# Optimization experiments

Hardware: AMD Instinct MI355X
Metric: run time of the kernel (lower is better)

## Reference

```python
import jax, jax.numpy as jnp
import numpy as np

B, D, N = 131072, 512, 101
BIG = 1e9
NORM_EPS = 0.1  # F.normalize eps


def setup_inputs() -> dict:
    key = jax.random.key(0)
    k1, k2, k3 = jax.random.split(key, 3)
    embeddings = jax.random.normal(k1, (B, D), dtype=jnp.float32)
    centers_weight = jax.random.normal(k2, (N, D), dtype=jnp.float32)
    labels = jax.random.randint(k3, (B,), 0, N, dtype=jnp.int64)
    return {"embeddings": embeddings, "centers_weight": centers_weight, "labels": labels}


def reference(embeddings, centers_weight, labels):
    # ---- center (MSE) term: per-sample squared distance to own center ----
    gathered = centers_weight[labels]                     # [B, D]
    center_loss = ((embeddings - gathered) ** 2).sum(axis=1)  # [B] (reduction=None)

    # ---- margin term (original operates on .data -> detached) ----
    W = jax.lax.stop_gradient(centers_weight)
    norms = jnp.sqrt((W * W).sum(axis=1, keepdims=True))
    C = W / jnp.maximum(norms, NORM_EPS)                  # F.normalize(p=2, eps=0.1)
    n = C.shape[0]
    dist = 1.0 - C @ C.T                                  # [N, N] cosine distance
    idx = jnp.arange(n)
    diff = jnp.abs(idx[:, None] - idx[None, :])
    dist = dist + BIG * (diff == 0)                       # mask diagonal (eye)

    # neighbor distances BEFORE they are masked out
    d_lower = jnp.diagonal(dist, offset=-1)               # Dist[i, i-1], i = 1..n-1
    d_upper = jnp.diagonal(dist, offset=1)                # Dist[i, i+1], i = 0..n-2

    dist_masked = dist + BIG * (diff == 1)                # mask adjacent centers
    min_dist = dist_masked.min(axis=1)                    # Dist[i, NegIdx]

    margin = (jax.nn.relu(2.0 * d_lower - min_dist[1:]).sum()
              + jax.nn.relu(2.0 * d_upper - min_dist[:-1]).sum()) / n

    return margin + center_loss.mean()
```

## Files before the change

kernel.cpp:

```cpp
#include <hip/hip_runtime.h>

#define BB 131072
#define DD 512
#define NN 101
#define D4 128
#define HALF 64
#define NBLK 256
#define BTHR 1024
#define SPB 1024
#define NPAIR (NN * NN)
#define PPB 80

typedef float f4 __attribute__((ext_vector_type(4)));

__global__ __launch_bounds__(BTHR, 1) void fused_kernel(
    const f4* __restrict__ emb, const f4* __restrict__ ctr,
    const int* __restrict__ labels,
    float* __restrict__ partial,
    float* __restrict__ G0,
    float* __restrict__ G1)
{
    __shared__ f4  sctr[NN * HALF];
    __shared__ int slab[SPB];
    __shared__ float wsum[16];

    int b    = blockIdx.x;
    int h    = b >> 7;
    int blk  = b & 127;
    int tid  = threadIdx.x;
    int wid  = tid >> 6;
    int lane = tid & 63;

    for (int idx = tid; idx < NN * HALF; idx += BTHR) {
        int row = idx >> 6;
        int c   = idx & 63;
        sctr[idx] = ctr[row * D4 + h * HALF + c];
    }
    slab[tid] = labels[blk * SPB + tid];
    __syncthreads();

    float* Gh = h ? G1 : G0;
#pragma unroll
    for (int rep = 0; rep < 5; rep++) {
        int p = blk * PPB + rep * 16 + wid;
        if (p < NPAIR) {
            int i = p / NN;
            int j = p % NN;
            f4 a = sctr[i * HALF + lane];
            f4 c = sctr[j * HALF + lane];
            float dot = a.x * c.x + a.y * c.y + a.z * c.z + a.w * c.w;
            for (int off = 32; off > 0; off >>= 1)
                dot += __shfl_down(dot, off);
            if (lane == 0) Gh[p] = dot;
        }
    }

    float local = 0.f;
#pragma unroll 1
    for (int kk = 0; kk < 16; kk++) {
        int q0 = (kk * 4 + 0) * 16 + wid;
        int q1 = (kk * 4 + 1) * 16 + wid;
        int q2 = (kk * 4 + 2) * 16 + wid;
        int q3 = (kk * 4 + 3) * 16 + wid;
        int l0 = slab[q0];
        int l1 = slab[q1];
        int l2 = slab[q2];
        int l3 = slab[q3];
        const f4* base = emb + h * HALF + lane;
        f4 e0 = __builtin_nontemporal_load(base + (blk * SPB + q0) * D4);
        f4 e1 = __builtin_nontemporal_load(base + (blk * SPB + q1) * D4);
        f4 e2 = __builtin_nontemporal_load(base + (blk * SPB + q2) * D4);
        f4 e3 = __builtin_nontemporal_load(base + (blk * SPB + q3) * D4);
        f4 c0 = sctr[l0 * HALF + lane];
        f4 c1 = sctr[l1 * HALF + lane];
        f4 c2 = sctr[l2 * HALF + lane];
        f4 c3 = sctr[l3 * HALF + lane];
        f4 t0 = e0 - c0;
        f4 t1 = e1 - c1;
        f4 t2 = e2 - c2;
        f4 t3 = e3 - c3;
        local += t0.x * t0.x + t0.y * t0.y + t0.z * t0.z + t0.w * t0.w;
        local += t1.x * t1.x + t1.y * t1.y + t1.z * t1.z + t1.w * t1.w;
        local += t2.x * t2.x + t2.y * t2.y + t2.z * t2.z + t2.w * t2.w;
        local += t3.x * t3.x + t3.y * t3.y + t3.z * t3.z + t3.w * t3.w;
    }
    for (int off = 32; off > 0; off >>= 1)
        local += __shfl_down(local, off);
    if (lane == 0) wsum[wid] = local;
    __syncthreads();
    if (tid == 0) {
        float s = 0.f;
#pragma unroll
        for (int w = 0; w < 16; w++) s += wsum[w];
        partial[b] = s;
    }
}

__global__ __launch_bounds__(256) void finalize_kernel(
    const float* __restrict__ G0, const float* __restrict__ G1,
    const float* __restrict__ partial, float* __restrict__ out)
{
    int t = threadIdx.x;

    double dsum = (t < NBLK) ? (double)partial[t] : 0.0;
    for (int off = 32; off > 0; off >>= 1)
        dsum += __shfl_down(dsum, off);
    __shared__ double dacc[4];
    if ((t & 63) == 0) dacc[t >> 6] = dsum;

    __shared__ float denom[NN];
    __shared__ float mind[NN];
    if (t < NN)
        denom[t] = fmaxf(sqrtf(G0[t * NN + t] + G1[t * NN + t]), 0.1f);
    __syncthreads();
    if (t < NN) {
        float di = denom[t];
        float mn = 1e30f;
        for (int j = 0; j < NN; j++) {
            if (j >= t - 1 && j <= t + 1) continue;
            float g = G0[t * NN + j] + G1[t * NN + j];
            float d = 1.0f - g / (di * denom[j]);
            mn = fminf(mn, d);
        }
        mind[t] = mn;
    }
    __syncthreads();
    float contrib = 0.f;
    if (t >= 1 && t < NN) {
        float g = G0[t * NN + (t - 1)] + G1[t * NN + (t - 1)];
        float dl = 1.0f - g / (denom[t] * denom[t - 1]);
        contrib += fmaxf(2.0f * dl - mind[t], 0.0f);
    }
    if (t < NN - 1) {
        float g = G0[t * NN + (t + 1)] + G1[t * NN + (t + 1)];
        float du = 1.0f - g / (denom[t] * denom[t + 1]);
        contrib += fmaxf(2.0f * du - mind[t], 0.0f);
    }
    for (int off = 32; off > 0; off >>= 1)
        contrib += __shfl_down(contrib, off);
    __shared__ float wsum2[4];
    if ((t & 63) == 0) wsum2[t >> 6] = contrib;
    __syncthreads();
    if (t == 0) {
        float margin = (wsum2[0] + wsum2[1] + wsum2[2] + wsum2[3]) / (float)NN;
        double center = (dacc[0] + dacc[1] + dacc[2] + dacc[3]) / (double)BB;
        out[0] = margin + (float)center;
    }
}

extern "C" void kernel_launch(void* const* d_in, const int* in_sizes, int n_in,
                              void* d_out, int out_size, void* d_ws, size_t ws_size,
                              hipStream_t stream) {
    const float* emb    = (const float*)d_in[0];
    const float* ctr    = (const float*)d_in[1];
    const int*   labels = (const int*)d_in[2];
    float* out = (float*)d_out;

    float* partial = (float*)d_ws;
    float* G0      = (float*)((char*)d_ws + 1024);
    float* G1      = G0 + NPAIR;

    fused_kernel<<<NBLK, BTHR, 0, stream>>>(
        (const f4*)emb, (const f4*)ctr, labels, partial, G0, G1);
    finalize_kernel<<<1, 256, 0, stream>>>(G0, G1, partial, out);
}
```

Measured before the change: 80.54 us.

## Fold finalize into main kernel via last-block atomic counter; reorder center loop first

Removes the second kernel launch by having each block atomically increment a counter after writing its partial sum and Gram entries; the last block to arrive runs the margin and final reduction. The streaming center-loss loop is also moved ahead of the Gram dot products so the global loads are issued earlier. This saves a launch and the gap between kernels, at the cost of extra fences and an atomic per block. The counter relies on wrapping modulo 256 across calls because it is never reset.

```diff
diff --git a/kernel.cpp b/kernel.cpp
--- a/kernel.cpp
+++ b/kernel.cpp
@@ -18,11 +18,18 @@
     const int* __restrict__ labels,
     float* __restrict__ partial,
     float* __restrict__ G0,
-    float* __restrict__ G1)
+    float* __restrict__ G1,
+    unsigned int* __restrict__ done,
+    float* __restrict__ out)
 {
     __shared__ f4  sctr[NN * HALF];
     __shared__ int slab[SPB];
     __shared__ float wsum[16];
+    __shared__ unsigned int gate;
+    __shared__ double dacc[4];
+    __shared__ float denom[NN];
+    __shared__ float mind[NN];
+    __shared__ float wsum2[16];
 
     int b    = blockIdx.x;
     int h    = b >> 7;
@@ -31,13 +38,40 @@
     int wid  = tid >> 6;
     int lane = tid & 63;
 
-    for (int idx = tid; idx < NN * HALF; idx += BTHR) {
-        int row = idx >> 6;
-        int c   = idx & 63;
-        sctr[idx] = ctr[row * D4 + h * HALF + c];
-    }
+    for (int idx = tid; idx < NN * HALF; idx += BTHR)
+        sctr[idx] = ctr[(idx >> 6) * D4 + h * HALF + (idx & 63)];
     slab[tid] = labels[blk * SPB + tid];
     __syncthreads();
+
+    float local = 0.f;
+    const f4* base = emb + h * HALF + lane;
+#pragma unroll 1
+    for (int kk = 0; kk < 16; kk++) {
+        int q0 = (kk * 4 + 0) * 16 + wid;
+        int q1 = (kk * 4 + 1) * 16 + wid;
+        int q2 = (kk * 4 + 2) * 16 + wid;
+        int q3 = (kk * 4 + 3) * 16 + wid;
+        int l0 = slab[q0];
+        int l1 = slab[q1];
+        int l2 = slab[q2];
+        int l3 = slab[q3];
+        f4 e0 = __builtin_nontemporal_load(base + (blk * SPB + q0) * D4);
+        f4 e1 = __builtin_nontemporal_load(base + (blk * SPB + q1) * D4);
+        f4 e2 = __builtin_nontemporal_load(base + (blk * SPB + q2) * D4);
+        f4 e3 = __builtin_nontemporal_load(base + (blk * SPB + q3) * D4);
+        f4 c0 = sctr[l0 * HALF + lane];
+        f4 c1 = sctr[l1 * HALF + lane];
+        f4 c2 = sctr[l2 * HALF + lane];
+        f4 c3 = sctr[l3 * HALF + lane];
+        f4 t0 = e0 - c0;
+        f4 t1 = e1 - c1;
+        f4 t2 = e2 - c2;
+        f4 t3 = e3 - c3;
+        local += t0.x * t0.x + t0.y * t0.y + t0.z * t0.z + t0.w * t0.w;
+        local += t1.x * t1.x + t1.y * t1.y + t1.z * t1.z + t1.w * t1.w;
+        local += t2.x * t2.x + t2.y * t2.y + t2.z * t2.z + t2.w * t2.w;
+        local += t3.x * t3.x + t3.y * t3.y + t3.z * t3.z + t3.w * t3.w;
+    }
 
     float* Gh = h ? G1 : G0;
 #pragma unroll
@@ -55,35 +89,6 @@
         }
     }
 
-    float local = 0.f;
-#pragma unroll 1
-    for (int kk = 0; kk < 16; kk++) {
-        int q0 = (kk * 4 + 0) * 16 + wid;
-        int q1 = (kk * 4 + 1) * 16 + wid;
-        int q2 = (kk * 4 + 2) * 16 + wid;
-        int q3 = (kk * 4 + 3) * 16 + wid;
-        int l0 = slab[q0];
-        int l1 = slab[q1];
-        int l2 = slab[q2];
-        int l3 = slab[q3];
-        const f4* base = emb + h * HALF + lane;
-        f4 e0 = __builtin_nontemporal_load(base + (blk * SPB + q0) * D4);
-        f4 e1 = __builtin_nontemporal_load(base + (blk * SPB + q1) * D4);
-        f4 e2 = __builtin_nontemporal_load(base + (blk * SPB + q2) * D4);
-        f4 e3 = __builtin_nontemporal_load(base + (blk * SPB + q3) * D4);
-        f4 c0 = sctr[l0 * HALF + lane];
-        f4 c1 = sctr[l1 * HALF + lane];
-        f4 c2 = sctr[l2 * HALF + lane];
-        f4 c3 = sctr[l3 * HALF + lane];
-        f4 t0 = e0 - c0;
-        f4 t1 = e1 - c1;
-        f4 t2 = e2 - c2;
-        f4 t3 = e3 - c3;
-        local += t0.x * t0.x + t0.y * t0.y + t0.z * t0.z + t0.w * t0.w;
-        local += t1.x * t1.x + t1.y * t1.y + t1.z * t1.z + t1.w * t1.w;
-        local += t2.x * t2.x + t2.y * t2.y + t2.z * t2.z + t2.w * t2.w;
-        local += t3.x * t3.x + t3.y * t3.y + t3.z * t3.z + t3.w * t3.w;
-    }
     for (int off = 32; off > 0; off >>= 1)
         local += __shfl_down(local, off);
     if (lane == 0) wsum[wid] = local;
@@ -94,22 +99,21 @@
         for (int w = 0; w < 16; w++) s += wsum[w];
         partial[b] = s;
     }
-}
 
-__global__ __launch_bounds__(256) void finalize_kernel(
-    const float* __restrict__ G0, const float* __restrict__ G1,
-    const float* __restrict__ partial, float* __restrict__ out)
-{
-    int t = threadIdx.x;
+    __threadfence();
+    __syncthreads();
+    if (tid == 0) gate = atomicAdd(done, 1u) & 255u;
+    __syncthreads();
+    if (gate != 255u) return;
+
+    __threadfence();
+    int t = tid;
 
     double dsum = (t < NBLK) ? (double)partial[t] : 0.0;
     for (int off = 32; off > 0; off >>= 1)
         dsum += __shfl_down(dsum, off);
-    __shared__ double dacc[4];
-    if ((t & 63) == 0) dacc[t >> 6] = dsum;
+    if (t < NBLK && (t & 63) == 0) dacc[t >> 6] = dsum;
 
-    __shared__ float denom[NN];
-    __shared__ float mind[NN];
     if (t < NN)
         denom[t] = fmaxf(sqrtf(G0[t * NN + t] + G1[t * NN + t]), 0.1f);
     __syncthreads();
@@ -119,8 +123,7 @@
         for (int j = 0; j < NN; j++) {
             if (j >= t - 1 && j <= t + 1) continue;
             float g = G0[t * NN + j] + G1[t * NN + j];
-            float d = 1.0f - g / (di * denom[j]);
-            mn = fminf(mn, d);
+            mn = fminf(mn, 1.0f - g / (di * denom[j]));
         }
         mind[t] = mn;
     }
@@ -128,21 +131,21 @@
     float contrib = 0.f;
     if (t >= 1 && t < NN) {
         float g = G0[t * NN + (t - 1)] + G1[t * NN + (t - 1)];
-        float dl = 1.0f - g / (denom[t] * denom[t - 1]);
-        contrib += fmaxf(2.0f * dl - mind[t], 0.0f);
+        contrib += fmaxf(2.0f * (1.0f - g / (denom[t] * denom[t - 1])) - mind[t], 0.0f);
     }
     if (t < NN - 1) {
         float g = G0[t * NN + (t + 1)] + G1[t * NN + (t + 1)];
-        float du = 1.0f - g / (denom[t] * denom[t + 1]);
-        contrib += fmaxf(2.0f * du - mind[t], 0.0f);
+        contrib += fmaxf(2.0f * (1.0f - g / (denom[t] * denom[t + 1])) - mind[t], 0.0f);
     }
     for (int off = 32; off > 0; off >>= 1)
         contrib += __shfl_down(contrib, off);
-    __shared__ float wsum2[4];
     if ((t & 63) == 0) wsum2[t >> 6] = contrib;
     __syncthreads();
     if (t == 0) {
-        float margin = (wsum2[0] + wsum2[1] + wsum2[2] + wsum2[3]) / (float)NN;
+        float margin = 0.f;
+#pragma unroll
+        for (int w = 0; w < 16; w++) margin += wsum2[w];
+        margin /= (float)NN;
         double center = (dacc[0] + dacc[1] + dacc[2] + dacc[3]) / (double)BB;
         out[0] = margin + (float)center;
     }
@@ -156,11 +159,11 @@
     const int*   labels = (const int*)d_in[2];
     float* out = (float*)d_out;
 
-    float* partial = (float*)d_ws;
-    float* G0      = (float*)((char*)d_ws + 1024);
-    float* G1      = G0 + NPAIR;
+    unsigned int* done = (unsigned int*)d_ws;
+    float* partial     = (float*)((char*)d_ws + 64);
+    float* G0          = (float*)((char*)d_ws + 64 + NBLK * 4);
+    float* G1          = G0 + NPAIR;
 
     fused_kernel<<<NBLK, BTHR, 0, stream>>>(
-        (const f4*)emb, (const f4*)ctr, labels, partial, G0, G1);
-    finalize_kernel<<<1, 256, 0, stream>>>(G0, G1, partial, out);
+        (const f4*)emb, (const f4*)ctr, labels, partial, G0, G1, done, out);
 }
```

Result: slower. 137.7 us (+71.0%).
